# Kernel tuning notes

Measured on AMD Instinct MI355X. Metric: run time of the kernel, lower is better.

The kernel has to match this reference:

```python
import jax, jax.numpy as jnp
import numpy as np

BN_EPS = 1e-5


def setup_inputs() -> dict:
    key = jax.random.key(0)
    ks = jax.random.split(key, 10)
    B, L, V, D = 4096, 200, 100000, 256
    tokens = jax.random.randint(ks[0], (B, L), 0, V, dtype=jnp.int32)
    lengths = jnp.maximum(jax.random.randint(ks[1], (B,), 0, L + 1, dtype=jnp.int32), 1)
    t = (jax.random.uniform(ks[2], (B,)) > 0.5).astype(jnp.float32)
    emb_table = jax.random.normal(ks[3], (V, D), dtype=jnp.float32)
    W1 = jax.random.normal(ks[4], (D, D), dtype=jnp.float32) * (1.0 / np.sqrt(D))
    b1 = jnp.zeros((D,), dtype=jnp.float32)
    gamma = jnp.ones((D,), dtype=jnp.float32)
    beta = jnp.zeros((D,), dtype=jnp.float32)
    w2 = jax.random.normal(ks[5], (D,), dtype=jnp.float32) * (1.0 / np.sqrt(D))
    b2 = jnp.zeros((), dtype=jnp.float32)
    return {"tokens": tokens, "lengths": lengths, "t": t, "emb_table": emb_table,
            "W1": W1, "b1": b1, "gamma": gamma, "beta": beta, "w2": w2, "b2": b2}


def reference(tokens, lengths, t, emb_table, W1, b1, gamma, beta, w2, b2):
    B, L = tokens.shape
    # ragged gather + mean pool (EmbeddingBag-mean equivalent)
    emb = emb_table[tokens]                                   # [B, L, D]
    mask = (jnp.arange(L)[None, :] < lengths[:, None]).astype(emb.dtype)  # [B, L]
    pooled = jnp.einsum('bld,bl->bd', emb, mask) / lengths[:, None].astype(emb.dtype)
    # fc_hidden -> BatchNorm1d (training-mode batch stats) -> ReLU (dropout = eval identity)
    z = pooled @ W1.T + b1                                    # [B, D]
    mu = jnp.mean(z, axis=0)
    var = jnp.var(z, axis=0)
    zn = (z - mu) / jnp.sqrt(var + BN_EPS)
    h = jax.nn.relu(gamma * zn + beta)
    # fc_output -> logits
    logits = h @ w2 + b2                                      # [B]
    # BCEWithLogitsLoss (mean, numerically stable)
    loss = jnp.mean(jnp.maximum(logits, 0.0) - logits * t + jnp.log1p(jnp.exp(-jnp.abs(logits))))
    return (loss, logits)
```

## Files before the change

### kernel.cpp

```cpp
#include <hip/hip_runtime.h>
#include <math.h>

#define B_ 4096
#define L_ 200
#define D_ 256

__global__ __launch_bounds__(256) void pool_kernel(
    const int* __restrict__ tokens, const int* __restrict__ lengths,
    const float* __restrict__ emb, float* __restrict__ pooled) {
  const int tid = threadIdx.x;
  const int wv = tid >> 6, lane = tid & 63;
  const int b = blockIdx.x * 4 + wv;
  const int len = lengths[b];
  const int* trow = tokens + b * L_;
  const float4* embv = (const float4*)emb;
  float4 a0 = make_float4(0.f, 0.f, 0.f, 0.f);
  float4 a1 = a0, a2 = a0, a3 = a0;
  for (int l0 = 0; l0 < len; l0 += 64) {
    int nt = len - l0; nt = nt > 64 ? 64 : nt;
    int tk = (lane < nt) ? trow[l0 + lane] : 0;
    int j = 0;
    for (; j + 4 <= nt; j += 4) {
      int t0 = __shfl(tk, j);
      int t1 = __shfl(tk, j + 1);
      int t2 = __shfl(tk, j + 2);
      int t3 = __shfl(tk, j + 3);
      float4 v0 = embv[(size_t)t0 * 64 + lane];
      float4 v1 = embv[(size_t)t1 * 64 + lane];
      float4 v2 = embv[(size_t)t2 * 64 + lane];
      float4 v3 = embv[(size_t)t3 * 64 + lane];
      a0.x += v0.x; a0.y += v0.y; a0.z += v0.z; a0.w += v0.w;
      a1.x += v1.x; a1.y += v1.y; a1.z += v1.z; a1.w += v1.w;
      a2.x += v2.x; a2.y += v2.y; a2.z += v2.z; a2.w += v2.w;
      a3.x += v3.x; a3.y += v3.y; a3.z += v3.z; a3.w += v3.w;
    }
    for (; j < nt; j++) {
      int t0 = __shfl(tk, j);
      float4 v0 = embv[(size_t)t0 * 64 + lane];
      a0.x += v0.x; a0.y += v0.y; a0.z += v0.z; a0.w += v0.w;
    }
  }
  const float inv = 1.0f / (float)len;
  float4 r;
  r.x = (a0.x + a1.x + a2.x + a3.x) * inv;
  r.y = (a0.y + a1.y + a2.y + a3.y) * inv;
  r.z = (a0.z + a1.z + a2.z + a3.z) * inv;
  r.w = (a0.w + a1.w + a2.w + a3.w) * inv;
  ((float4*)pooled)[(size_t)b * 64 + lane] = r;
}

__global__ __launch_bounds__(256) void w1_pack_kernel(const float* __restrict__ W1,
                                                      float* __restrict__ W1p) {
  int kb = blockIdx.x;
  int d = threadIdx.x;
  float4 v = ((const float4*)W1)[d * 64 + kb];
  ((float4*)W1p)[kb * 256 + d] = v;
}

__global__ __launch_bounds__(256) void gemm_z_kernel(
    const float* __restrict__ pooled, const float* __restrict__ W1p,
    const float* __restrict__ b1, float* __restrict__ z) {
  __shared__ float4 P4[16 * 64];
  const int tid = threadIdx.x;
  const int b0 = blockIdx.x * 16;
  const float4* pooled4 = (const float4*)pooled;
#pragma unroll
  for (int i = 0; i < 4; i++)
    P4[tid + i * 256] = pooled4[(size_t)b0 * 64 + tid + i * 256];
  __syncthreads();
  const int wv = tid >> 6, lane = tid & 63;
  const int r0 = wv * 4;
  float4 bb = ((const float4*)b1)[lane];
  float acc[4][4];
#pragma unroll
  for (int r = 0; r < 4; r++) {
    acc[r][0] = bb.x; acc[r][1] = bb.y; acc[r][2] = bb.z; acc[r][3] = bb.w;
  }
  const float4* w4 = (const float4*)W1p;
  for (int kb = 0; kb < 64; kb++) {
    float4 wk0 = w4[kb * 256 + lane * 4 + 0];
    float4 wk1 = w4[kb * 256 + lane * 4 + 1];
    float4 wk2 = w4[kb * 256 + lane * 4 + 2];
    float4 wk3 = w4[kb * 256 + lane * 4 + 3];
#pragma unroll
    for (int r = 0; r < 4; r++) {
      float4 p = P4[(r0 + r) * 64 + kb];
      acc[r][0] += p.x * wk0.x + p.y * wk0.y + p.z * wk0.z + p.w * wk0.w;
      acc[r][1] += p.x * wk1.x + p.y * wk1.y + p.z * wk1.z + p.w * wk1.w;
      acc[r][2] += p.x * wk2.x + p.y * wk2.y + p.z * wk2.z + p.w * wk2.w;
      acc[r][3] += p.x * wk3.x + p.y * wk3.y + p.z * wk3.z + p.w * wk3.w;
    }
  }
  float4* z4 = (float4*)z;
#pragma unroll
  for (int r = 0; r < 4; r++) {
    float4 o = make_float4(acc[r][0], acc[r][1], acc[r][2], acc[r][3]);
    z4[(size_t)(b0 + r0 + r) * 64 + lane] = o;
  }
}

__global__ __launch_bounds__(256) void stats_kernel(const float* __restrict__ z,
                                                    float* __restrict__ ssum,
                                                    float* __restrict__ ssq) {
  const int d = threadIdx.x;
  const int r0 = blockIdx.x * 64;
  float s = 0.f, q = 0.f;
  for (int i = 0; i < 64; i++) {
    float v = z[(size_t)(r0 + i) * 256 + d];
    s += v; q += v * v;
  }
  atomicAdd(&ssum[d], s);
  atomicAdd(&ssq[d], q);
}

__global__ __launch_bounds__(256) void head_kernel(
    const float* __restrict__ z, const float* __restrict__ ssum,
    const float* __restrict__ ssq, const float* __restrict__ gamma,
    const float* __restrict__ beta, const float* __restrict__ w2,
    const float* __restrict__ b2, const float* __restrict__ t,
    float* __restrict__ out, float* __restrict__ bce) {
  const int tid = threadIdx.x;
  const int wv = tid >> 6, lane = tid & 63;
  const int b = blockIdx.x * 4 + wv;
  float4 s4 = ((const float4*)ssum)[lane];
  float4 q4 = ((const float4*)ssq)[lane];
  float4 g4 = ((const float4*)gamma)[lane];
  float4 be4 = ((const float4*)beta)[lane];
  float4 w24 = ((const float4*)w2)[lane];
  const float invB = 1.0f / 4096.0f;
  float4 A4, C4;
  {
    float m = s4.x * invB, v = q4.x * invB - m * m;
    float rs = rsqrtf(v + 1e-5f); A4.x = g4.x * rs; C4.x = be4.x - m * A4.x;
  }
  {
    float m = s4.y * invB, v = q4.y * invB - m * m;
    float rs = rsqrtf(v + 1e-5f); A4.y = g4.y * rs; C4.y = be4.y - m * A4.y;
  }
  {
    float m = s4.z * invB, v = q4.z * invB - m * m;
    float rs = rsqrtf(v + 1e-5f); A4.z = g4.z * rs; C4.z = be4.z - m * A4.z;
  }
  {
    float m = s4.w * invB, v = q4.w * invB - m * m;
    float rs = rsqrtf(v + 1e-5f); A4.w = g4.w * rs; C4.w = be4.w - m * A4.w;
  }
  float4 zv = ((const float4*)z)[(size_t)b * 64 + lane];
  float h0 = fmaxf(A4.x * zv.x + C4.x, 0.f);
  float h1 = fmaxf(A4.y * zv.y + C4.y, 0.f);
  float h2 = fmaxf(A4.z * zv.z + C4.z, 0.f);
  float h3 = fmaxf(A4.w * zv.w + C4.w, 0.f);
  float part = h0 * w24.x + h1 * w24.y + h2 * w24.z + h3 * w24.w;
#pragma unroll
  for (int off = 32; off > 0; off >>= 1) part += __shfl_down(part, off);
  if (lane == 0) {
    float logit = part + b2[0];
    out[1 + b] = logit;
    float tb = t[b];
    bce[b] = fmaxf(logit, 0.f) - logit * tb + log1pf(expf(-fabsf(logit)));
  }
}

__global__ __launch_bounds__(256) void loss_kernel(const float* __restrict__ bce,
                                                   float* __restrict__ out) {
  __shared__ float red[4];
  const int tid = threadIdx.x;
  float s = 0.f;
  for (int i = 0; i < 16; i++) s += bce[tid + i * 256];
#pragma unroll
  for (int off = 32; off > 0; off >>= 1) s += __shfl_down(s, off);
  if ((tid & 63) == 0) red[tid >> 6] = s;
  __syncthreads();
  if (tid == 0) out[0] = (red[0] + red[1] + red[2] + red[3]) * (1.0f / 4096.0f);
}

extern "C" void kernel_launch(void* const* d_in, const int* in_sizes, int n_in,
                              void* d_out, int out_size, void* d_ws, size_t ws_size,
                              hipStream_t stream) {
  const int* tokens = (const int*)d_in[0];
  const int* lengths = (const int*)d_in[1];
  const float* t = (const float*)d_in[2];
  const float* emb = (const float*)d_in[3];
  const float* W1 = (const float*)d_in[4];
  const float* b1 = (const float*)d_in[5];
  const float* gamma = (const float*)d_in[6];
  const float* beta = (const float*)d_in[7];
  const float* w2 = (const float*)d_in[8];
  const float* b2 = (const float*)d_in[9];
  float* out = (float*)d_out;

  float* wsf = (float*)d_ws;
  float* pooled = wsf;
  float* z = wsf + 1048576;
  float* W1p = wsf + 2097152;
  float* ssum = wsf + 2162688;
  float* ssq = wsf + 2162944;
  float* bce = wsf + 2163200;

  hipMemsetAsync(ssum, 0, 512 * sizeof(float), stream);
  w1_pack_kernel<<<64, 256, 0, stream>>>(W1, W1p);
  pool_kernel<<<1024, 256, 0, stream>>>(tokens, lengths, emb, pooled);
  gemm_z_kernel<<<256, 256, 0, stream>>>(pooled, W1p, b1, z);
  stats_kernel<<<64, 256, 0, stream>>>(z, ssum, ssq);
  head_kernel<<<1024, 256, 0, stream>>>(z, ssum, ssq, gamma, beta, w2, b2, t, out, bce);
  loss_kernel<<<1, 256, 0, stream>>>(bce, out);
}
```

Baseline: 244.1 us.

## Split pooling rows across two waves and fuse BN stats into GEMM

The W1 pack moves into the pooling kernel, and each batch row's gather is split across two waves with a shared-memory combine, doubling the grid to 2048 blocks. Column sum and sum-of-squares are computed in the GEMM epilogue as per-block partials, which replaces the separate z re-read and the atomics. A small reduce kernel turns the partials into BN scale and shift, and the memset is dropped. The aim is fewer launches, more memory-level parallelism in the gather, and no second pass over z, at the cost of an extra barrier in pooling and one more small kernel.

```diff
diff --git a/kernel.cpp b/kernel.cpp
--- a/kernel.cpp
+++ b/kernel.cpp
@@ -1,22 +1,26 @@
 #include <hip/hip_runtime.h>
 #include <math.h>
 
-#define B_ 4096
 #define L_ 200
-#define D_ 256
-
-__global__ __launch_bounds__(256) void pool_kernel(
+
+__global__ __launch_bounds__(256) void pool_pack_kernel(
     const int* __restrict__ tokens, const int* __restrict__ lengths,
-    const float* __restrict__ emb, float* __restrict__ pooled) {
-  const int tid = threadIdx.x;
+    const float* __restrict__ emb, float* __restrict__ pooled,
+    const float* __restrict__ W1, float* __restrict__ W1p) {
+  const int tid = threadIdx.x;
+  if (blockIdx.x < 64) {
+    float4 v = ((const float4*)W1)[tid * 64 + blockIdx.x];
+    ((float4*)W1p)[blockIdx.x * 256 + tid] = v;
+  }
   const int wv = tid >> 6, lane = tid & 63;
-  const int b = blockIdx.x * 4 + wv;
-  const int len = lengths[b];
-  const int* trow = tokens + b * L_;
+  const int row = blockIdx.x * 2 + (wv >> 1);
+  const int half = wv & 1;
+  const int len = lengths[row];
+  const int* trow = tokens + row * L_;
   const float4* embv = (const float4*)emb;
   float4 a0 = make_float4(0.f, 0.f, 0.f, 0.f);
   float4 a1 = a0, a2 = a0, a3 = a0;
-  for (int l0 = 0; l0 < len; l0 += 64) {
+  for (int l0 = half * 64; l0 < len; l0 += 128) {
     int nt = len - l0; nt = nt > 64 ? 64 : nt;
     int tk = (lane < nt) ? trow[l0 + lane] : 0;
     int j = 0;
@@ -40,33 +44,36 @@
       a0.x += v0.x; a0.y += v0.y; a0.z += v0.z; a0.w += v0.w;
     }
   }
-  const float inv = 1.0f / (float)len;
   float4 r;
-  r.x = (a0.x + a1.x + a2.x + a3.x) * inv;
-  r.y = (a0.y + a1.y + a2.y + a3.y) * inv;
-  r.z = (a0.z + a1.z + a2.z + a3.z) * inv;
-  r.w = (a0.w + a1.w + a2.w + a3.w) * inv;
-  ((float4*)pooled)[(size_t)b * 64 + lane] = r;
-}
-
-__global__ __launch_bounds__(256) void w1_pack_kernel(const float* __restrict__ W1,
-                                                      float* __restrict__ W1p) {
-  int kb = blockIdx.x;
-  int d = threadIdx.x;
-  float4 v = ((const float4*)W1)[d * 64 + kb];
-  ((float4*)W1p)[kb * 256 + d] = v;
-}
-
-__global__ __launch_bounds__(256) void gemm_z_kernel(
+  r.x = a0.x + a1.x + a2.x + a3.x;
+  r.y = a0.y + a1.y + a2.y + a3.y;
+  r.z = a0.z + a1.z + a2.z + a3.z;
+  r.w = a0.w + a1.w + a2.w + a3.w;
+  __shared__ float4 part[2][64];
+  if (half) part[wv >> 1][lane] = r;
+  __syncthreads();
+  if (!half) {
+    float4 o = part[wv >> 1][lane];
+    const float inv = 1.0f / (float)len;
+    r.x = (r.x + o.x) * inv;
+    r.y = (r.y + o.y) * inv;
+    r.z = (r.z + o.z) * inv;
+    r.w = (r.w + o.w) * inv;
+    ((float4*)pooled)[(size_t)row * 64 + lane] = r;
+  }
+}
+
+__global__ __launch_bounds__(256) void gemm_stats_kernel(
     const float* __restrict__ pooled, const float* __restrict__ W1p,
-    const float* __restrict__ b1, float* __restrict__ z) {
-  __shared__ float4 P4[16 * 64];
+    const float* __restrict__ b1, float* __restrict__ z,
+    float* __restrict__ psum, float* __restrict__ psq) {
+  __shared__ float4 SH[1024];
   const int tid = threadIdx.x;
   const int b0 = blockIdx.x * 16;
   const float4* pooled4 = (const float4*)pooled;
 #pragma unroll
   for (int i = 0; i < 4; i++)
-    P4[tid + i * 256] = pooled4[(size_t)b0 * 64 + tid + i * 256];
+    SH[tid + i * 256] = pooled4[(size_t)b0 * 64 + tid + i * 256];
   __syncthreads();
   const int wv = tid >> 6, lane = tid & 63;
   const int r0 = wv * 4;
@@ -84,7 +91,7 @@
     float4 wk3 = w4[kb * 256 + lane * 4 + 3];
 #pragma unroll
     for (int r = 0; r < 4; r++) {
-      float4 p = P4[(r0 + r) * 64 + kb];
+      float4 p = SH[(r0 + r) * 64 + kb];
       acc[r][0] += p.x * wk0.x + p.y * wk0.y + p.z * wk0.z + p.w * wk0.w;
       acc[r][1] += p.x * wk1.x + p.y * wk1.y + p.z * wk1.z + p.w * wk1.w;
       acc[r][2] += p.x * wk2.x + p.y * wk2.y + p.z * wk2.z + p.w * wk2.w;
@@ -92,59 +99,73 @@
     }
   }
   float4* z4 = (float4*)z;
+  float4 s = make_float4(0.f, 0.f, 0.f, 0.f), q = s;
 #pragma unroll
   for (int r = 0; r < 4; r++) {
     float4 o = make_float4(acc[r][0], acc[r][1], acc[r][2], acc[r][3]);
     z4[(size_t)(b0 + r0 + r) * 64 + lane] = o;
-  }
-}
-
-__global__ __launch_bounds__(256) void stats_kernel(const float* __restrict__ z,
-                                                    float* __restrict__ ssum,
-                                                    float* __restrict__ ssq) {
-  const int d = threadIdx.x;
-  const int r0 = blockIdx.x * 64;
+    s.x += o.x; s.y += o.y; s.z += o.z; s.w += o.w;
+    q.x += o.x * o.x; q.y += o.y * o.y; q.z += o.z * o.z; q.w += o.w * o.w;
+  }
+  __syncthreads();
+  SH[wv * 64 + lane] = s;
+  SH[256 + wv * 64 + lane] = q;
+  __syncthreads();
+  if (tid < 64) {
+    float4 S = make_float4(0.f, 0.f, 0.f, 0.f), Q = S;
+#pragma unroll
+    for (int w = 0; w < 4; w++) {
+      float4 a = SH[w * 64 + tid];
+      float4 b = SH[256 + w * 64 + tid];
+      S.x += a.x; S.y += a.y; S.z += a.z; S.w += a.w;
+      Q.x += b.x; Q.y += b.y; Q.z += b.z; Q.w += b.w;
+    }
+    ((float4*)psum)[blockIdx.x * 64 + tid] = S;
+    ((float4*)psq)[blockIdx.x * 64 + tid] = Q;
+  }
+}
+
+__global__ __launch_bounds__(256) void bn_reduce_kernel(
+    const float* __restrict__ psum, const float* __restrict__ psq,
+    const float* __restrict__ gamma, const float* __restrict__ beta,
+    float* __restrict__ A, float* __restrict__ C) {
+  const int t = threadIdx.x;
+  const int dd = t & 15, c = t >> 4;
+  const int d = blockIdx.x * 16 + dd;
   float s = 0.f, q = 0.f;
-  for (int i = 0; i < 64; i++) {
-    float v = z[(size_t)(r0 + i) * 256 + d];
-    s += v; q += v * v;
-  }
-  atomicAdd(&ssum[d], s);
-  atomicAdd(&ssq[d], q);
+#pragma unroll
+  for (int i = 0; i < 16; i++) {
+    int p = c * 16 + i;
+    s += psum[p * 256 + d];
+    q += psq[p * 256 + d];
+  }
+  __shared__ float sl[16][17], ql[16][17];
+  sl[c][dd] = s; ql[c][dd] = q;
+  __syncthreads();
+  if (t < 16) {
+    float S = 0.f, Q = 0.f;
+#pragma unroll
+    for (int c2 = 0; c2 < 16; c2++) { S += sl[c2][t]; Q += ql[c2][t]; }
+    int dg = blockIdx.x * 16 + t;
+    float m = S * (1.0f / 4096.0f);
+    float v = Q * (1.0f / 4096.0f) - m * m;
+    float a = gamma[dg] * rsqrtf(v + 1e-5f);
+    A[dg] = a;
+    C[dg] = beta[dg] - m * a;
+  }
 }
 
 __global__ __launch_bounds__(256) void head_kernel(
-    const float* __restrict__ z, const float* __restrict__ ssum,
-    const float* __restrict__ ssq, const float* __restrict__ gamma,
-    const float* __restrict__ beta, const float* __restrict__ w2,
+    const float* __restrict__ z, const float* __restrict__ A,
+    const float* __restrict__ C, const float* __restrict__ w2,
     const float* __restrict__ b2, const float* __restrict__ t,
     float* __restrict__ out, float* __restrict__ bce) {
   const int tid = threadIdx.x;
   const int wv = tid >> 6, lane = tid & 63;
   const int b = blockIdx.x * 4 + wv;
-  float4 s4 = ((const float4*)ssum)[lane];
-  float4 q4 = ((const float4*)ssq)[lane];
-  float4 g4 = ((const float4*)gamma)[lane];
-  float4 be4 = ((const float4*)beta)[lane];
+  float4 A4 = ((const float4*)A)[lane];
+  float4 C4 = ((const float4*)C)[lane];
   float4 w24 = ((const float4*)w2)[lane];
-  const float invB = 1.0f / 4096.0f;
-  float4 A4, C4;
-  {
-    float m = s4.x * invB, v = q4.x * invB - m * m;
-    float rs = rsqrtf(v + 1e-5f); A4.x = g4.x * rs; C4.x = be4.x - m * A4.x;
-  }
-  {
-    float m = s4.y * invB, v = q4.y * invB - m * m;
-    float rs = rsqrtf(v + 1e-5f); A4.y = g4.y * rs; C4.y = be4.y - m * A4.y;
-  }
-  {
-    float m = s4.z * invB, v = q4.z * invB - m * m;
-    float rs = rsqrtf(v + 1e-5f); A4.z = g4.z * rs; C4.z = be4.z - m * A4.z;
-  }
-  {
-    float m = s4.w * invB, v = q4.w * invB - m * m;
-    float rs = rsqrtf(v + 1e-5f); A4.w = g4.w * rs; C4.w = be4.w - m * A4.w;
-  }
   float4 zv = ((const float4*)z)[(size_t)b * 64 + lane];
   float h0 = fmaxf(A4.x * zv.x + C4.x, 0.f);
   float h1 = fmaxf(A4.y * zv.y + C4.y, 0.f);
@@ -193,15 +214,15 @@
   float* pooled = wsf;
   float* z = wsf + 1048576;
   float* W1p = wsf + 2097152;
-  float* ssum = wsf + 2162688;
-  float* ssq = wsf + 2162944;
-  float* bce = wsf + 2163200;
-
-  hipMemsetAsync(ssum, 0, 512 * sizeof(float), stream);
-  w1_pack_kernel<<<64, 256, 0, stream>>>(W1, W1p);
-  pool_kernel<<<1024, 256, 0, stream>>>(tokens, lengths, emb, pooled);
-  gemm_z_kernel<<<256, 256, 0, stream>>>(pooled, W1p, b1, z);
-  stats_kernel<<<64, 256, 0, stream>>>(z, ssum, ssq);
-  head_kernel<<<1024, 256, 0, stream>>>(z, ssum, ssq, gamma, beta, w2, b2, t, out, bce);
+  float* psum = wsf + 2162688;
+  float* psq = wsf + 2228224;
+  float* A = wsf + 2293760;
+  float* C = wsf + 2294016;
+  float* bce = wsf + 2294272;
+
+  pool_pack_kernel<<<2048, 256, 0, stream>>>(tokens, lengths, emb, pooled, W1, W1p);
+  gemm_stats_kernel<<<256, 256, 0, stream>>>(pooled, W1p, b1, z, psum, psq);
+  bn_reduce_kernel<<<16, 256, 0, stream>>>(psum, psq, gamma, beta, A, C);
+  head_kernel<<<1024, 256, 0, stream>>>(z, A, C, w2, b2, t, out, bce);
   loss_kernel<<<1, 256, 0, stream>>>(bce, out);
 }
```

Measured after the change: 240.8 us. Within noise of the previous version (-1.3%).
